# Performance work log

Hardware: AMD Instinct MI355X
Metric: run time of the kernel (lower is better)

## Reference

```python
import jax, jax.numpy as jnp
import numpy as np

S0 = 100.0
V0 = 0.04
RATE = 0.025
MC = 50000          # MC_samples; 2*MC antithetic paths
N_STEPS = 180       # == int(x[:,0].max()), pinned in setup_inputs for static shapes
WIDTH = 64
N_OPTS = 32
H = 1.0 / 360.0     # timegrid step: (maxT/360)/maxT


def setup_inputs():
    key = jax.random.key(0)
    ks = jax.random.split(key, 8)
    mat = jax.random.randint(ks[0], (N_OPTS,), 30, N_STEPS + 1).astype(jnp.float32)
    mat = mat.at[0].set(float(N_STEPS))  # pin max maturity -> static n_steps
    strikes = 80.0 + 40.0 * jax.random.uniform(ks[1], (N_OPTS,), dtype=jnp.float32)
    x = jnp.stack([mat, strikes], axis=1)  # [n_opts, 2]: (maturity_days, strike)
    z = jax.random.normal(ks[2], (MC, N_STEPS), dtype=jnp.float32)
    z1 = jax.random.normal(ks[3], (MC, N_STEPS), dtype=jnp.float32)
    # 4 stacked tiny MLPs: order = [driftS, diffusionS, driftV, diffusionV]
    W1 = 0.1 * jax.random.normal(ks[4], (4, WIDTH, 4), dtype=jnp.float32)
    b1 = jnp.zeros((4, WIDTH), jnp.float32)
    W2 = 0.1 * jax.random.normal(ks[5], (4, WIDTH, WIDTH), dtype=jnp.float32)
    b2 = jnp.zeros((4, WIDTH), jnp.float32)
    Wo = 0.05 * jax.random.normal(ks[6], (4, 1, WIDTH), dtype=jnp.float32)
    bo = jnp.zeros((4, 1), jnp.float32)
    return dict(x=x, z=z, z1=z1, W1=W1, b1=b1, W2=W2, b2=b2, Wo=Wo, bo=bo)


def _mlp4(inp, W1, b1, W2, b2, Wo, bo):
    # Evaluate the 4 tiny MLPs on the shared input [M,4] in one batched pass.
    h1 = jax.nn.relu(jnp.einsum('nwd,md->nmw', W1, inp) + b1[:, None, :])
    h2 = jax.nn.relu(jnp.einsum('nvw,nmw->nmv', W2, h1) + b2[:, None, :])
    out = jnp.einsum('now,nmw->nmo', Wo, h2) + bo[:, None, :]
    return out[..., 0]  # [4, M]


def _forward(x, z, z1, W1, b1, W2, b2, Wo, bo, remat=False):
    M = 2 * MC
    h = jnp.float32(H)
    sqh = jnp.sqrt(h)
    # correlated second Brownian: z1 <- -0.5*z + sqrt(0.75)*z1, then antithetic
    z1c = -0.5 * z + np.float32(np.sqrt(0.75)) * z1
    zf = jnp.concatenate([z, -z], axis=0)        # [M, T]
    z1f = jnp.concatenate([z1c, -z1c], axis=0)   # [M, T]
    tgrid = jnp.arange(N_STEPS, dtype=jnp.float32) * h  # t_{i-1}
    rate_col = jnp.full((M,), RATE, jnp.float32)

    def step(carry, xs):
        S, V = carry
        zc, z1cc, tc = xs
        dW = sqh * zc
        dW1 = sqh * z1cc
        inp = jnp.stack([jnp.full((M,), tc), S, V, rate_col], axis=1)  # [M,4]
        o = _mlp4(inp, W1, b1, W2, b2, Wo, bo)  # [4, M]
        Sn = jnp.maximum(S + o[0] * h + o[1] * dW, 0.0)   # max(., 0) clamp
        Vn = jnp.maximum(V + o[2] * h + o[3] * dW1, 0.0)
        return (Sn, Vn), Sn

    if remat:
        step = jax.checkpoint(step)
    init = (jnp.full((M,), S0, jnp.float32), jnp.full((M,), V0, jnp.float32))
    _, Spath = jax.lax.scan(step, init, (zf.T, z1f.T, tgrid))  # Spath: [T, M]
    Sample_path = jnp.concatenate([jnp.full((1, M), S0, jnp.float32), Spath], axis=0)  # [T+1, M]

    # vectorized option pricing over all rows of x
    idx = x[:, 0].astype(jnp.int32)                  # maturity index into path
    ST = Sample_path[idx]                            # [n_opts, M]
    payoff = jnp.maximum(ST - x[:, 1][:, None], 0.0)
    price = payoff.mean(axis=1) * jnp.exp(-RATE * x[:, 0] / 360.0)
    return price.reshape(-1, 1)


def reference(x, z, z1, W1, b1, W2, b2, Wo, bo):
    return _forward(x, z, z1, W1, b1, W2, b2, Wo, bo, remat=False)
```

## Files before the change

kernel.cpp:

```cpp
#include <hip/hip_runtime.h>
#include <math.h>

#define MC      50000
#define MPATHS  100000
#define NSTEPS  180
#define NOPTS   32

typedef __attribute__((ext_vector_type(8))) short short8;
typedef __attribute__((ext_vector_type(4))) float float4v;
typedef __attribute__((ext_vector_type(4))) unsigned u32x4;
typedef _Float16 half2v __attribute__((ext_vector_type(2)));
typedef unsigned u32x32 __attribute__((ext_vector_type(32)));

static __device__ __forceinline__ unsigned bf16u(float x) {
    unsigned u = __float_as_uint(x);
    return (u + 0x7fffu + ((u >> 16) & 1u)) >> 16;
}
static __device__ __forceinline__ float bf16val(float x) {
    return __uint_as_float(bf16u(x) << 16);
}
static __device__ __forceinline__ unsigned pkh2(float a, float b) {
    half2v h; h.x = (_Float16)a; h.y = (_Float16)b;
    return __builtin_bit_cast(unsigned, h);
}
static __device__ __forceinline__ unsigned pkrtz(float a, float b) {
    auto h = __builtin_amdgcn_cvt_pkrtz(a, b);
    return __builtin_bit_cast(unsigned, h);
}
static __device__ __forceinline__ float fdot2(unsigned w, unsigned h, float c) {
    return __builtin_amdgcn_fdot2(__builtin_bit_cast(half2v, w),
                                  __builtin_bit_cast(half2v, h), c, false);
}
static __device__ __forceinline__ short8 fr4(unsigned a, unsigned b,
                                             unsigned c, unsigned d) {
    union { unsigned u[4]; short8 s; } t;
    t.u[0] = a; t.u[1] = b; t.u[2] = c; t.u[3] = d;
    return t.s;
}
static __device__ __forceinline__ float4v mfma16(short8 a, short8 b, float4v c) {
    return __builtin_amdgcn_mfma_f32_16x16x32_bf16(a, b, c, 0, 0, 0);
}


__global__ void probe_mn(int* tbl) {
    const int lane = threadIdx.x;
    for (int s = lane; s < 2048; s += 64) tbl[s] = 0;
    const float4v z4 = {0.f, 0.f, 0.f, 0.f};
    for (int L = 0; L < 64; ++L)
        for (int j = 0; j < 8; ++j) {
            unsigned au[4] = {0u, 0u, 0u, 0u};
            if (lane == L) au[j >> 1] = 0x3F80u << (16 * (j & 1));
            short8 a = fr4(au[0], au[1], au[2], au[3]);
            short8 b = fr4(0x3F803F80u, 0x3F803F80u, 0x3F803F80u, 0x3F803F80u);
            float4v d = mfma16(a, b, z4);
            if ((lane & 15) == 0) {
                #pragma unroll
                for (int r = 0; r < 4; ++r)
                    if (d[r] != 0.0f) tbl[L * 8 + j] = (lane >> 4) * 4 + r;
            }
        }
    for (int L = 0; L < 64; ++L)
        for (int j = 0; j < 8; ++j) {
            unsigned bu[4] = {0u, 0u, 0u, 0u};
            if (lane == L) bu[j >> 1] = 0x3F80u << (16 * (j & 1));
            short8 a = fr4(0x3F803F80u, 0x3F803F80u, 0x3F803F80u, 0x3F803F80u);
            short8 b = fr4(bu[0], bu[1], bu[2], bu[3]);
            float4v d = mfma16(a, b, z4);
            if ((lane >> 4) == 0 && d[0] != 0.0f) tbl[1024 + L * 8 + j] = (lane & 15);
        }
}

__global__ void probe_k(int* tbl) {
    const int lane = threadIdx.x;
    const int sA = blockIdx.x;
    const float4v z4 = {0.f, 0.f, 0.f, 0.f};
    unsigned au[4] = {0u, 0u, 0u, 0u};
    if (lane == (sA >> 3)) au[(sA & 7) >> 1] = 0x3F80u << (16 * (sA & 1));
    short8 a = fr4(au[0], au[1], au[2], au[3]);
    int kid = -1;
    for (int sB = 0; sB < 512; ++sB) {
        unsigned bu[4] = {0u, 0u, 0u, 0u};
        const int LB = sB >> 3, jB = sB & 7;
        if (lane == LB) bu[jB >> 1] = 0x3F80u << (16 * (jB & 1));
        short8 b = fr4(bu[0], bu[1], bu[2], bu[3]);
        float4v d = mfma16(a, b, z4);
        bool hit = (d[0] != 0.f) | (d[1] != 0.f) | (d[2] != 0.f) | (d[3] != 0.f);
        if (__any(hit)) {
            if (kid < 0) kid = sB;
            if (lane == 0) tbl[1536 + sB] = kid;
        }
    }
    if (lane == 0) tbl[512 + sA] = (kid < 0) ? 0 : kid;
}

__global__ void finalize_verify(int* tbl, int* flag) {
    __shared__ int cnt[32];
    __shared__ int minv[32];
    const int lane = threadIdx.x;
    if (lane < 32) { cnt[lane] = 0; minv[lane] = 0; }
    int rA[8], rB[8];
    #pragma unroll
    for (int j = 0; j < 8; ++j) {
        const int s = lane * 8 + j;
        const int kidA = tbl[512 + s], kidB = tbl[1536 + s];
        int ra = 0, rb = 0;
        for (int u = 0; u < 512; ++u) {
            const int canon = (tbl[1536 + u] == u);
            ra += canon & (u < kidA);
            rb += canon & (u < kidB);
        }
        rA[j] = ra & 31; rB[j] = rb & 31;
    }
    __syncthreads();
    #pragma unroll
    for (int j = 0; j < 8; ++j) {
        tbl[512 + lane * 8 + j]  = rA[j];
        tbl[1536 + lane * 8 + j] = rB[j];
    }
    unsigned au[4] = {0u, 0u, 0u, 0u}, bu[4] = {0u, 0u, 0u, 0u};
    #pragma unroll
    for (int j = 0; j < 8; ++j) {
        const int s = lane * 8 + j;
        const int m = tbl[s] & 15, ka = rA[j];
        const int n = tbl[1024 + s] & 15, kb = rB[j];
        const int fv = ((m * 7 + ka * 3) % 5) - 2;
        const int gv = ((kb * 5 + n * 11) % 7) - 3;
        au[j >> 1] |= bf16u((float)fv) << (16 * (j & 1));
        bu[j >> 1] |= bf16u((float)gv) << (16 * (j & 1));
    }
    const float4v z4 = {0.f, 0.f, 0.f, 0.f};
    float4v d = mfma16(fr4(au[0], au[1], au[2], au[3]),
                       fr4(bu[0], bu[1], bu[2], bu[3]), z4);
    const int col = lane & 15;
    bool ok = true;
    #pragma unroll
    for (int r = 0; r < 4; ++r) {
        const int row = (lane >> 4) * 4 + r;
        int ref = 0;
        for (int k = 0; k < 32; ++k)
            ref += (((row * 7 + k * 3) % 5) - 2) * (((k * 5 + col * 11) % 7) - 3);
        ok = ok && (d[r] == (float)ref);
    }
    bool okf = ok;
    #pragma unroll
    for (int j = 0; j < 8; ++j) {
        okf = okf && ((tbl[1024 + lane * 8 + j] & 15) == (lane & 15));
        const int ref = __shfl(rB[j], lane & 48, 64);
        okf = okf && (rB[j] == ref);
    }
    if ((lane & 15) == 0) {
        const int g = lane >> 4;
        #pragma unroll
        for (int j = 0; j < 8; ++j) {
            atomicAdd(&cnt[rB[j]], 1);
            minv[rB[j]] = 16 * ((j >> 2) & 1) + 4 * g + 2 * ((j >> 1) & 1) + (j & 1);
        }
    }
    __syncthreads();
    if (lane < 32) {
        okf = okf && (cnt[lane] == 1);
        tbl[2048 + lane] = minv[lane];
    }
    const bool allok = __all(okf);
    if (lane == 0) *flag = allok ? 1 : 0;
}

__global__ void build_frags(const float* __restrict__ W1, const float* __restrict__ b1,
                            const float* __restrict__ W2, const float* __restrict__ Wo,
                            const int* __restrict__ tbl,
                            uint4* __restrict__ w1f, uint4* __restrict__ w2f,
                            uint4* __restrict__ w3f) {
    const int t = blockIdx.x * 256 + threadIdx.x;
    if (t >= 3584) return;
    const int lane = t & 63, frag = t >> 6;
    const float rateB = bf16val(0.025f);
    unsigned u[4] = {0u, 0u, 0u, 0u};
    if (frag < 16) {
        const int net = frag >> 2, mt = frag & 3;
        #pragma unroll
        for (int j = 0; j < 8; ++j) {
            const int s = lane * 8 + j;
            const int m = tbl[s] & 15, k = tbl[512 + s] & 31;
            unsigned bits = 0u;
            if (k < 12) {
                const int kk = (k < 6) ? k : k - 6;
                const int M = net * 64 + 16 * mt + m;
                float v;
                if (kk == 0)                 v = W1[M * 4 + 0];
                else if (kk == 1 || kk == 4) v = W1[M * 4 + 1];
                else if (kk == 2 || kk == 5) v = W1[M * 4 + 2];
                else                         v = W1[M * 4 + 3] + b1[M] / rateB;
                bits = (k < 6) ? bf16u(v) : bf16u(v - bf16val(v));
            }
            u[j >> 1] |= bits << (16 * (j & 1));
        }
        w1f[frag * 64 + lane] = make_uint4(u[0], u[1], u[2], u[3]);
    } else if (frag < 48) {
        const int f2 = frag - 16;
        const int net = f2 >> 3, mt = (f2 >> 1) & 3, kc = f2 & 1;
        #pragma unroll
        for (int j = 0; j < 8; ++j) {
            const int s = lane * 8 + j;
            const int m = tbl[s] & 15, k = tbl[512 + s] & 31;
            const float v = W2[(net * 64 + 16 * mt + m) * 64 + 32 * kc + tbl[2048 + k]];
            u[j >> 1] |= bf16u(v) << (16 * (j & 1));
        }
        w2f[f2 * 64 + lane] = make_uint4(u[0], u[1], u[2], u[3]);
    } else {
        const int f3 = frag - 48;
        const int net = f3 >> 1, kc = f3 & 1;
        #pragma unroll
        for (int j = 0; j < 8; ++j) {
            const int s = lane * 8 + j;
            const int k = tbl[512 + s] & 31;
            const float v = Wo[net * 64 + 32 * kc + tbl[2048 + k]];
            u[j >> 1] |= bf16u(v) << (16 * (j & 1));
        }
        w3f[f3 * 64 + lane] = make_uint4(u[0], u[1], u[2], u[3]);
    }
}

__global__ __launch_bounds__(256, 3)
void sde_mfma_w4(const float* __restrict__ x, const float* __restrict__ z,
                 const float* __restrict__ z1, const float* __restrict__ b2,
                 const float* __restrict__ bo,
                 const int* __restrict__ tbl, const uint4* __restrict__ w1f,
                 const uint4* __restrict__ w2f, const uint4* __restrict__ w3f,
                 const int* __restrict__ flag, float* __restrict__ acc)
{
    if (*flag != 1) return;
    __shared__ __align__(16) float b2_s[256];
    __shared__ float dxch[2][4][64];
    __shared__ float ls_k[NOPTS];
    __shared__ int   maskTab[NSTEPS + 4];

    const int tid = threadIdx.x;
    const int wv = tid >> 6, lane = tid & 63;
    const int q = lane >> 4, c = lane & 15;

    for (int j = tid; j < 256; j += 256) b2_s[j] = b2[j];
    for (int j = tid; j < NSTEPS + 4; j += 256) maskTab[j] = 0;
    if (tid < NOPTS) ls_k[tid] = x[2 * tid + 1];
    __syncthreads();
    if (tid < NOPTS) atomicOr(&maskTab[(int)x[2 * tid]], 1 << tid);
    __syncthreads();

    const unsigned rate16 = bf16u(0.025f);
    unsigned selAB[4], dynM[4], cU[4], mT[4];
    {
        int rowj[8];
        #pragma unroll
        for (int j = 0; j < 8; ++j) {
            const int kb = tbl[1536 + lane * 8 + j] & 31;
            rowj[j] = (kb < 6) ? kb : ((kb < 12) ? kb - 6 : 6);
        }
        #pragma unroll
        for (int w = 0; w < 4; ++w) {
            unsigned s = 0, d = 0, cu = 0, mt_ = 0;
            #pragma unroll
            for (int h = 0; h < 2; ++h) {
                const int r = rowj[2 * w + h];
                unsigned hs = 0x0504u, hd = 0u, hcu = 0u, hmt = 0u;
                if      (r == 1) { hs = 0x0504u; hd = 0xFFFFu; }
                else if (r == 2) { hs = 0x0706u; hd = 0xFFFFu; }
                else if (r == 4) { hs = 0x0100u; hd = 0xFFFFu; }
                else if (r == 5) { hs = 0x0302u; hd = 0xFFFFu; }
                else if (r == 0) { hmt = 0xFFFFu; }
                else if (r == 3) { hcu = rate16; }
                s  |= hs  << (16 * h); d   |= hd  << (16 * h);
                cu |= hcu << (16 * h); mt_ |= hmt << (16 * h);
            }
            selAB[w] = s; dynM[w] = d; cU[w] = cu; mT[w] = mt_;
        }
    }

    const int p_ = blockIdx.x * 64 + lane;
    const float wgt = (p_ < MPATHS) ? 1.0f : 0.0f;
    int pc = (p_ < MPATHS) ? p_ : (MPATHS - 1);
    float sgn = 1.0f; int row_ = pc;
    if (pc >= MC) { sgn = -1.0f; row_ -= MC; }
    const float* __restrict__ zrow  = z  + (size_t)row_ * NSTEPS;
    const float* __restrict__ z1row = z1 + (size_t)row_ * NSTEPS;

    const float hh = 1.0f / 360.0f, sqh = sqrtf(hh);
    const float s75 = 0.86602540378443864676f;
    const float bon = bo[wv];

    const u32x4* __restrict__ w1v = (const u32x4*)w1f;
    const u32x4* __restrict__ w2v = (const u32x4*)w2f;
    const u32x4* __restrict__ w3v = (const u32x4*)w3f;
    u32x4 a1v[4], a2v[8];
    #pragma unroll
    for (int mt = 0; mt < 4; ++mt) {
        a1v[mt]         = w1v[(wv * 4 + mt) * 64 + lane];
        a2v[2 * mt]     = w2v[((wv * 4 + mt) * 2 + 0) * 64 + lane];
        a2v[2 * mt + 1] = w2v[((wv * 4 + mt) * 2 + 1) * 64 + lane];
    }
    const u32x4 a3v0 = w3v[(wv * 2 + 0) * 64 + lane];
    const u32x4 a3v1 = w3v[(wv * 2 + 1) * 64 + lane];
    float4v c4r[4];
    #pragma unroll
    for (int mt = 0; mt < 4; ++mt)
        c4r[mt] = *(const float4v*)&b2_s[wv * 64 + 16 * mt + 4 * q];

    float S = 100.0f, V = 0.04f;

    const bool needZ  = (wv == 1) | (wv == 3);
    const bool needZ1 = (wv == 3);
    float4 zc = {0.f, 0.f, 0.f, 0.f}, z1c = {0.f, 0.f, 0.f, 0.f};
    float4 zn = zc, z1n = z1c;
    if (needZ)  zc  = *(const float4*)(zrow);
    if (needZ1) z1c = *(const float4*)(z1row);

    #pragma unroll 1
    for (int ch = 0; ch < NSTEPS / 4; ++ch) {
        if (ch + 1 < NSTEPS / 4) {
            if (needZ)  zn  = *(const float4*)(zrow  + 4 * (ch + 1));
            if (needZ1) z1n = *(const float4*)(z1row + 4 * (ch + 1));
        }
        #pragma unroll
        for (int ii = 0; ii < 4; ++ii) {
            const int i = 4 * ch + ii;
            const float zz  = (ii == 0) ? zc.x  : (ii == 1) ? zc.y  : (ii == 2) ? zc.z  : zc.w;
            const float zz1 = (ii == 0) ? z1c.x : (ii == 1) ? z1c.y : (ii == 2) ? z1c.z : z1c.w;
            float mult;
            if      (wv == 1) mult = sqh * (sgn * zz);
            else if (wv == 3) mult = sqh * (sgn * (-0.5f * zz + s75 * zz1));
            else              mult = hh;

            const float t = (float)i * hh;
            const unsigned tB = bf16u(t);
            const unsigned tB2 = tB | (tB << 16);
            unsigned UW[4];
            #pragma unroll
            for (int w = 0; w < 4; ++w) UW[w] = cU[w] | (mT[w] & tB2);

            const unsigned Shu = bf16u(S), Vhu = bf16u(V);
            const unsigned PA = Shu | (Vhu << 16);
            const float Sr = S - __uint_as_float(Shu << 16);
            const float Vr = V - __uint_as_float(Vhu << 16);
            const unsigned PB = __builtin_amdgcn_perm(__float_as_uint(Vr),
                                                      __float_as_uint(Sr), 0x07060302u);

            float osel = 0.0f;
            #pragma unroll
            for (int nt = 0; nt < 4; ++nt) {
                const int a = (nt << 6) | (c << 2);
                const unsigned Ap = (unsigned)__builtin_amdgcn_ds_bpermute(a, (int)PA);
                const unsigned Bp = (unsigned)__builtin_amdgcn_ds_bpermute(a, (int)PB);
                u32x4 b1v;
                b1v.x = (__builtin_amdgcn_perm(Ap, Bp, selAB[0]) & dynM[0]) | UW[0];
                b1v.y = (__builtin_amdgcn_perm(Ap, Bp, selAB[1]) & dynM[1]) | UW[1];
                b1v.z = (__builtin_amdgcn_perm(Ap, Bp, selAB[2]) & dynM[2]) | UW[2];
                b1v.w = (__builtin_amdgcn_perm(Ap, Bp, selAB[3]) & dynM[3]) | UW[3];
                const short8 B1s = __builtin_bit_cast(short8, b1v);

                const float4v z4 = {0.f, 0.f, 0.f, 0.f};
                u32x4 bk0, bk1;
                #pragma unroll
                for (int mt = 0; mt < 4; ++mt) {
                    float4v d = mfma16(__builtin_bit_cast(short8, a1v[mt]), B1s, z4);
                    const unsigned r0 = __float_as_uint(fmaxf(d[0], 0.f));
                    const unsigned r1 = __float_as_uint(fmaxf(d[1], 0.f));
                    const unsigned r2 = __float_as_uint(fmaxf(d[2], 0.f));
                    const unsigned r3 = __float_as_uint(fmaxf(d[3], 0.f));
                    const unsigned plo = __builtin_amdgcn_perm(r1, r0, 0x07060302u);
                    const unsigned phi = __builtin_amdgcn_perm(r3, r2, 0x07060302u);
                    if      (mt == 0) { bk0.x = plo; bk0.y = phi; }
                    else if (mt == 1) { bk0.z = plo; bk0.w = phi; }
                    else if (mt == 2) { bk1.x = plo; bk1.y = phi; }
                    else              { bk1.z = plo; bk1.w = phi; }
                }
                const short8 Bk0 = __builtin_bit_cast(short8, bk0);
                const short8 Bk1 = __builtin_bit_cast(short8, bk1);
                u32x4 hk0, hk1;
                #pragma unroll
                for (int mt = 0; mt < 4; ++mt) {
                    float4v d = mfma16(__builtin_bit_cast(short8, a2v[2 * mt]), Bk0, c4r[mt]);
                    d = mfma16(__builtin_bit_cast(short8, a2v[2 * mt + 1]), Bk1, d);
                    const unsigned r0 = __float_as_uint(fmaxf(d[0], 0.f));
                    const unsigned r1 = __float_as_uint(fmaxf(d[1], 0.f));
                    const unsigned r2 = __float_as_uint(fmaxf(d[2], 0.f));
                    const unsigned r3 = __float_as_uint(fmaxf(d[3], 0.f));
                    const unsigned plo = __builtin_amdgcn_perm(r1, r0, 0x07060302u);
                    const unsigned phi = __builtin_amdgcn_perm(r3, r2, 0x07060302u);
                    if      (mt == 0) { hk0.x = plo; hk0.y = phi; }
                    else if (mt == 1) { hk0.z = plo; hk0.w = phi; }
                    else if (mt == 2) { hk1.x = plo; hk1.y = phi; }
                    else              { hk1.z = plo; hk1.w = phi; }
                }
                float4v dO = mfma16(__builtin_bit_cast(short8, a3v0),
                                    __builtin_bit_cast(short8, hk0), z4);
                dO = mfma16(__builtin_bit_cast(short8, a3v1),
                            __builtin_bit_cast(short8, hk1), dO);
                if (nt == q) osel = dO[0];
            }
            const float o = osel + bon;

            dxch[i & 1][wv][lane] = o * mult;
            __syncthreads();
            const float dS = dxch[i & 1][0][lane] + dxch[i & 1][1][lane];
            const float dV = dxch[i & 1][2][lane] + dxch[i & 1][3][lane];
            S = fmaxf(S + dS, 0.0f);
            V = fmaxf(V + dV, 0.0f);

            if (wv == 0) {
                int mm = maskTab[i + 1];
                while (mm) {
                    const int qq = __ffs(mm) - 1; mm &= mm - 1;
                    float pay = wgt * fmaxf(S - ls_k[qq], 0.0f);
                    #pragma unroll
                    for (int off = 32; off > 0; off >>= 1)
                        pay += __shfl_down(pay, off, 64);
                    if (lane == 0) atomicAdd(&acc[qq], pay);
                }
            }
        }
        zc = zn; z1c = z1n;
    }
}

__global__ void pack_w(const float* __restrict__ W1, const float* __restrict__ W2,
                       unsigned* __restrict__ wp1, unsigned* __restrict__ wp2) {
    int i = blockIdx.x * 256 + threadIdx.x;
    if (i < 512)              wp1[i] = pkh2(W1[2 * i], W1[2 * i + 1]);
    else if (i < 512 + 8192) { int k = i - 512; wp2[k] = pkh2(W2[2 * k], W2[2 * k + 1]); }
}

__global__ __launch_bounds__(64, 2)
void sde_dot2(const float* __restrict__ x, const float* __restrict__ z,
              const float* __restrict__ z1, const float* __restrict__ b1,
              const float* __restrict__ b2, const float* __restrict__ Wo,
              const float* __restrict__ bo, const uint4* __restrict__ wp1,
              const uint4* __restrict__ wp2, const int* __restrict__ flag,
              float* __restrict__ acc)
{
    if (*flag == 1) return;
    __shared__ __align__(16) uint4 wlds[2176];
    __shared__ float ls_k[NOPTS];
    __shared__ int   maskTab[NSTEPS + 4];
    const int tid = threadIdx.x;
    for (int j = tid; j < 2176; j += 64) wlds[j] = (j < 128) ? wp1[j] : wp2[j - 128];
    for (int jj = tid; jj < NSTEPS + 4; jj += 64) maskTab[jj] = 0;
    if (tid < NOPTS) ls_k[tid] = x[2 * tid + 1];
    __syncthreads();
    if (tid < NOPTS) atomicOr(&maskTab[(int)x[2 * tid]], 1 << tid);
    __syncthreads();
    const int pA = blockIdx.x * 128 + tid, pB = pA + 64;
    const float wgtA = (pA < MPATHS) ? 1.0f : 0.0f;
    const float wgtB = (pB < MPATHS) ? 1.0f : 0.0f;
    int pcA = (pA < MPATHS) ? pA : (MPATHS - 1);
    int pcB = (pB < MPATHS) ? pB : (MPATHS - 1);
    float sgnA = 1.0f, sgnB = 1.0f; int rowA = pcA, rowB = pcB;
    if (pcA >= MC) { sgnA = -1.0f; rowA -= MC; }
    if (pcB >= MC) { sgnB = -1.0f; rowB -= MC; }
    const float* __restrict__ zA  = z  + (size_t)rowA * NSTEPS;
    const float* __restrict__ z1A = z1 + (size_t)rowA * NSTEPS;
    const float* __restrict__ zB  = z  + (size_t)rowB * NSTEPS;
    const float* __restrict__ z1B = z1 + (size_t)rowB * NSTEPS;
    const float hh = 1.0f / 360.0f, sqh = sqrtf(hh);
    const float s75 = 0.86602540378443864676f, rate = 0.025f;
    float SA = 100.0f, VA = 0.04f, SB = 100.0f, VB = 0.04f;
    #pragma unroll 1
    for (int i = 0; i < NSTEPS; ++i) {
        const float zcrA = zA[i], z1rA = z1A[i], zcrB = zB[i], z1rB = z1B[i];
        const float dWA = sqh * (sgnA * zcrA);
        const float dW1A = sqh * (sgnA * (-0.5f * zcrA + s75 * z1rA));
        const float dWB = sqh * (sgnB * zcrB);
        const float dW1B = sqh * (sgnB * (-0.5f * zcrB + s75 * z1rB));
        const float t = (float)i * hh;
        const unsigned inA01 = pkrtz(t, SA), inA23 = pkrtz(VA, rate);
        const unsigned inB01 = pkrtz(t, SB), inB23 = pkrtz(VB, rate);
        float dSA = 0.f, dVA = 0.f, dSB = 0.f, dVB = 0.f;
        #pragma unroll 1
        for (int net = 0; net < 4; ++net) {
            const float* __restrict__ b1n = b1 + net * 64;
            const float* __restrict__ b2n = b2 + net * 64;
            const float* __restrict__ won = Wo + net * 64;
            const uint4* __restrict__ wl1 = &wlds[net * 32];
            const uint4* __restrict__ wl2 = &wlds[128 + net * 512];
            u32x32 hA, hB;
            #pragma unroll
            for (int u = 0; u < 64; u += 2) {
                const uint4 wv = wl1[u >> 1];
                const float bb0 = b1n[u], bb1 = b1n[u + 1];
                float a0 = fdot2(wv.x, inA01, bb0); a0 = fdot2(wv.y, inA23, a0);
                float a1 = fdot2(wv.z, inA01, bb1); a1 = fdot2(wv.w, inA23, a1);
                float c0 = fdot2(wv.x, inB01, bb0); c0 = fdot2(wv.y, inB23, c0);
                float c1 = fdot2(wv.z, inB01, bb1); c1 = fdot2(wv.w, inB23, c1);
                hA[u >> 1] = pkrtz(fmaxf(a0, 0.f), fmaxf(a1, 0.f));
                hB[u >> 1] = pkrtz(fmaxf(c0, 0.f), fmaxf(c1, 0.f));
            }
            float outA = bo[net], outB = outA;
            #pragma unroll 1
            for (int j = 0; j < 64; j += 4) {
                const uint4* __restrict__ r0 = wl2 + (j + 0) * 8;
                const uint4* __restrict__ r1 = wl2 + (j + 1) * 8;
                const uint4* __restrict__ r2 = wl2 + (j + 2) * 8;
                const uint4* __restrict__ r3 = wl2 + (j + 3) * 8;
                float a0 = b2n[j], a1 = b2n[j + 1], a2 = b2n[j + 2], a3 = b2n[j + 3];
                float c0 = a0, c1 = a1, c2 = a2, c3 = a3;
                #pragma unroll
                for (int kk = 0; kk < 8; ++kk) {
                    const uint4 w0 = r0[kk], w1 = r1[kk], w2 = r2[kk], w3 = r3[kk];
                    const unsigned hA0 = hA[4 * kk], hA1 = hA[4 * kk + 1];
                    const unsigned hA2 = hA[4 * kk + 2], hA3 = hA[4 * kk + 3];
                    const unsigned hB0 = hB[4 * kk], hB1 = hB[4 * kk + 1];
                    const unsigned hB2 = hB[4 * kk + 2], hB3 = hB[4 * kk + 3];
                    a0 = fdot2(w0.x, hA0, a0); a0 = fdot2(w0.y, hA1, a0);
                    a0 = fdot2(w0.z, hA2, a0); a0 = fdot2(w0.w, hA3, a0);
                    a1 = fdot2(w1.x, hA0, a1); a1 = fdot2(w1.y, hA1, a1);
                    a1 = fdot2(w1.z, hA2, a1); a1 = fdot2(w1.w, hA3, a1);
                    a2 = fdot2(w2.x, hA0, a2); a2 = fdot2(w2.y, hA1, a2);
                    a2 = fdot2(w2.z, hA2, a2); a2 = fdot2(w2.w, hA3, a2);
                    a3 = fdot2(w3.x, hA0, a3); a3 = fdot2(w3.y, hA1, a3);
                    a3 = fdot2(w3.z, hA2, a3); a3 = fdot2(w3.w, hA3, a3);
                    c0 = fdot2(w0.x, hB0, c0); c0 = fdot2(w0.y, hB1, c0);
                    c0 = fdot2(w0.z, hB2, c0); c0 = fdot2(w0.w, hB3, c0);
                    c1 = fdot2(w1.x, hB0, c1); c1 = fdot2(w1.y, hB1, c1);
                    c1 = fdot2(w1.z, hB2, c1); c1 = fdot2(w1.w, hB3, c1);
                    c2 = fdot2(w2.x, hB0, c2); c2 = fdot2(w2.y, hB1, c2);
                    c2 = fdot2(w2.z, hB2, c2); c2 = fdot2(w2.w, hB3, c2);
                    c3 = fdot2(w3.x, hB0, c3); c3 = fdot2(w3.y, hB1, c3);
                    c3 = fdot2(w3.z, hB2, c3); c3 = fdot2(w3.w, hB3, c3);
                }
                const float wo0 = won[j], wo1 = won[j + 1];
                const float wo2 = won[j + 2], wo3 = won[j + 3];
                outA = fmaf(wo0, fmaxf(a0, 0.f), outA); outA = fmaf(wo1, fmaxf(a1, 0.f), outA);
                outA = fmaf(wo2, fmaxf(a2, 0.f), outA); outA = fmaf(wo3, fmaxf(a3, 0.f), outA);
                outB = fmaf(wo0, fmaxf(c0, 0.f), outB); outB = fmaf(wo1, fmaxf(c1, 0.f), outB);
                outB = fmaf(wo2, fmaxf(c2, 0.f), outB); outB = fmaf(wo3, fmaxf(c3, 0.f), outB);
            }
            const float msA = (net == 0) ? hh : (net == 1) ? dWA  : 0.0f;
            const float mvA = (net == 2) ? hh : (net == 3) ? dW1A : 0.0f;
            const float msB = (net == 0) ? hh : (net == 1) ? dWB  : 0.0f;
            const float mvB = (net == 2) ? hh : (net == 3) ? dW1B : 0.0f;
            dSA = fmaf(outA, msA, dSA); dVA = fmaf(outA, mvA, dVA);
            dSB = fmaf(outB, msB, dSB); dVB = fmaf(outB, mvB, dVB);
        }
        SA = fmaxf(SA + dSA, 0.f); VA = fmaxf(VA + dVA, 0.f);
        SB = fmaxf(SB + dSB, 0.f); VB = fmaxf(VB + dVB, 0.f);
        int mm = maskTab[i + 1];
        while (mm) {
            const int qq = __ffs(mm) - 1; mm &= mm - 1;
            float pay = wgtA * fmaxf(SA - ls_k[qq], 0.f) + wgtB * fmaxf(SB - ls_k[qq], 0.f);
            #pragma unroll
            for (int off = 32; off > 0; off >>= 1)
                pay += __shfl_down(pay, off, 64);
            if (tid == 0) atomicAdd(&acc[qq], pay);
        }
    }
}

__global__ void price_kernel(const float* __restrict__ x, const float* __restrict__ acc,
                             float* __restrict__ out) {
    const int q = threadIdx.x;
    if (q < NOPTS) {
        const float mat = x[q * 2];
        out[q] = acc[q] * (1.0f / (float)MPATHS) * expf((-0.025f * mat) / 360.0f);
    }
}

extern "C" void kernel_launch(void* const* d_in, const int* in_sizes, int n_in,
                              void* d_out, int out_size, void* d_ws, size_t ws_size,
                              hipStream_t stream)
{
    const float* x  = (const float*)d_in[0];
    const float* z  = (const float*)d_in[1];
    const float* z1 = (const float*)d_in[2];
    const float* W1 = (const float*)d_in[3];
    const float* b1 = (const float*)d_in[4];
    const float* W2 = (const float*)d_in[5];
    const float* b2 = (const float*)d_in[6];
    const float* Wo = (const float*)d_in[7];
    const float* bo = (const float*)d_in[8];

    char* ws = (char*)d_ws;
    float*    acc  = (float*)ws;
    int*      flag = (int*)(ws + 256);
    int*      tbl  = (int*)(ws + 1024);
    uint4*    w1f  = (uint4*)(ws + 16384);
    uint4*    w2f  = (uint4*)(ws + 32768);
    unsigned* wp1  = (unsigned*)(ws + 65536);
    unsigned* wp2  = wp1 + 512;
    uint4*    w3f  = (uint4*)(ws + 100352);

    (void)hipMemsetAsync(acc, 0, NOPTS * sizeof(float), stream);
    pack_w<<<(512 + 8192 + 255) / 256, 256, 0, stream>>>(W1, W2, wp1, wp2);
    probe_mn<<<1, 64, 0, stream>>>(tbl);
    probe_k<<<512, 64, 0, stream>>>(tbl);
    finalize_verify<<<1, 64, 0, stream>>>(tbl, flag);
    build_frags<<<14, 256, 0, stream>>>(W1, b1, W2, Wo, tbl, w1f, w2f, w3f);

    const int gridS = (MPATHS + 63) / 64;
    sde_mfma_w4<<<gridS, 256, 0, stream>>>(x, z, z1, b2, bo, tbl, w1f, w2f, w3f,
                                           flag, acc);
    const int gridF = (MPATHS + 127) / 128;
    sde_dot2<<<gridF, 64, 0, stream>>>(x, z, z1, b1, b2, Wo, bo,
                                       (const uint4*)wp1, (const uint4*)wp2, flag, acc);
    price_kernel<<<1, 64, 0, stream>>>(x, acc, (float*)d_out);
}
```

Baseline: 1.491 ms.

## Split MLP nets across two waves per block instead of four

Each block now runs 128 threads, and each wave evaluates two of the four MLP nets (drift and diffusion for S, or for V) rather than one net per wave. The combined increment is formed locally with an fma, and only two values are exchanged through shared memory per step. Weight fragments for layers 1 and 2 are now reloaded from global memory inside the step loop instead of being held in registers. This aims to cut barrier and cross-wave exchange cost and lower register pressure, at the cost of repeated weight loads and twice the serial MFMA work per wave.

```diff
diff --git a/kernel.cpp b/kernel.cpp
--- a/kernel.cpp
+++ b/kernel.cpp
@@ -220,8 +220,8 @@
     }
 }
 
-__global__ __launch_bounds__(256, 3)
-void sde_mfma_w4(const float* __restrict__ x, const float* __restrict__ z,
+__global__ __launch_bounds__(128, 3)
+void sde_mfma_p2(const float* __restrict__ x, const float* __restrict__ z,
                  const float* __restrict__ z1, const float* __restrict__ b2,
                  const float* __restrict__ bo,
                  const int* __restrict__ tbl, const uint4* __restrict__ w1f,
@@ -230,7 +230,7 @@
 {
     if (*flag != 1) return;
     __shared__ __align__(16) float b2_s[256];
-    __shared__ float dxch[2][4][64];
+    __shared__ float dxch[2][2][64];
     __shared__ float ls_k[NOPTS];
     __shared__ int   maskTab[NSTEPS + 4];
 
@@ -238,8 +238,8 @@
     const int wv = tid >> 6, lane = tid & 63;
     const int q = lane >> 4, c = lane & 15;
 
-    for (int j = tid; j < 256; j += 256) b2_s[j] = b2[j];
-    for (int j = tid; j < NSTEPS + 4; j += 256) maskTab[j] = 0;
+    for (int j = tid; j < 256; j += 128) b2_s[j] = b2[j];
+    for (int j = tid; j < NSTEPS + 4; j += 128) maskTab[j] = 0;
     if (tid < NOPTS) ls_k[tid] = x[2 * tid + 1];
     __syncthreads();
     if (tid < NOPTS) atomicOr(&maskTab[(int)x[2 * tid]], 1 << tid);
@@ -284,38 +284,27 @@
 
     const float hh = 1.0f / 360.0f, sqh = sqrtf(hh);
     const float s75 = 0.86602540378443864676f;
-    const float bon = bo[wv];
+    const float bo0 = bo[2 * wv], bo1 = bo[2 * wv + 1];
 
     const u32x4* __restrict__ w1v = (const u32x4*)w1f;
     const u32x4* __restrict__ w2v = (const u32x4*)w2f;
     const u32x4* __restrict__ w3v = (const u32x4*)w3f;
-    u32x4 a1v[4], a2v[8];
+    u32x4 a3[4];
     #pragma unroll
-    for (int mt = 0; mt < 4; ++mt) {
-        a1v[mt]         = w1v[(wv * 4 + mt) * 64 + lane];
-        a2v[2 * mt]     = w2v[((wv * 4 + mt) * 2 + 0) * 64 + lane];
-        a2v[2 * mt + 1] = w2v[((wv * 4 + mt) * 2 + 1) * 64 + lane];
-    }
-    const u32x4 a3v0 = w3v[(wv * 2 + 0) * 64 + lane];
-    const u32x4 a3v1 = w3v[(wv * 2 + 1) * 64 + lane];
-    float4v c4r[4];
-    #pragma unroll
-    for (int mt = 0; mt < 4; ++mt)
-        c4r[mt] = *(const float4v*)&b2_s[wv * 64 + 16 * mt + 4 * q];
+    for (int f = 0; f < 4; ++f) a3[f] = w3v[(wv * 4 + f) * 64 + lane];
 
     float S = 100.0f, V = 0.04f;
 
-    const bool needZ  = (wv == 1) | (wv == 3);
-    const bool needZ1 = (wv == 3);
-    float4 zc = {0.f, 0.f, 0.f, 0.f}, z1c = {0.f, 0.f, 0.f, 0.f};
+    const bool needZ1 = (wv == 1);
+    float4 zc  = *(const float4*)(zrow);
+    float4 z1c = {0.f, 0.f, 0.f, 0.f};
+    if (needZ1) z1c = *(const float4*)(z1row);
     float4 zn = zc, z1n = z1c;
-    if (needZ)  zc  = *(const float4*)(zrow);
-    if (needZ1) z1c = *(const float4*)(z1row);
 
     #pragma unroll 1
     for (int ch = 0; ch < NSTEPS / 4; ++ch) {
         if (ch + 1 < NSTEPS / 4) {
-            if (needZ)  zn  = *(const float4*)(zrow  + 4 * (ch + 1));
+            zn = *(const float4*)(zrow + 4 * (ch + 1));
             if (needZ1) z1n = *(const float4*)(z1row + 4 * (ch + 1));
         }
         #pragma unroll
@@ -323,10 +312,9 @@
             const int i = 4 * ch + ii;
             const float zz  = (ii == 0) ? zc.x  : (ii == 1) ? zc.y  : (ii == 2) ? zc.z  : zc.w;
             const float zz1 = (ii == 0) ? z1c.x : (ii == 1) ? z1c.y : (ii == 2) ? z1c.z : z1c.w;
-            float mult;
-            if      (wv == 1) mult = sqh * (sgn * zz);
-            else if (wv == 3) mult = sqh * (sgn * (-0.5f * zz + s75 * zz1));
-            else              mult = hh;
+            float m1;
+            if (wv) m1 = sqh * (sgn * (-0.5f * zz + s75 * zz1));
+            else    m1 = sqh * (sgn * zz);
 
             const float t = (float)i * hh;
             const unsigned tB = bf16u(t);
@@ -342,7 +330,7 @@
             const unsigned PB = __builtin_amdgcn_perm(__float_as_uint(Vr),
                                                       __float_as_uint(Sr), 0x07060302u);
 
-            float osel = 0.0f;
+            float osel0 = 0.0f, osel1 = 0.0f;
             #pragma unroll
             for (int nt = 0; nt < 4; ++nt) {
                 const int a = (nt << 6) | (c << 2);
@@ -354,53 +342,64 @@
                 b1v.z = (__builtin_amdgcn_perm(Ap, Bp, selAB[2]) & dynM[2]) | UW[2];
                 b1v.w = (__builtin_amdgcn_perm(Ap, Bp, selAB[3]) & dynM[3]) | UW[3];
                 const short8 B1s = __builtin_bit_cast(short8, b1v);
-
                 const float4v z4 = {0.f, 0.f, 0.f, 0.f};
-                u32x4 bk0, bk1;
+
                 #pragma unroll
-                for (int mt = 0; mt < 4; ++mt) {
-                    float4v d = mfma16(__builtin_bit_cast(short8, a1v[mt]), B1s, z4);
-                    const unsigned r0 = __float_as_uint(fmaxf(d[0], 0.f));
-                    const unsigned r1 = __float_as_uint(fmaxf(d[1], 0.f));
-                    const unsigned r2 = __float_as_uint(fmaxf(d[2], 0.f));
-                    const unsigned r3 = __float_as_uint(fmaxf(d[3], 0.f));
-                    const unsigned plo = __builtin_amdgcn_perm(r1, r0, 0x07060302u);
-                    const unsigned phi = __builtin_amdgcn_perm(r3, r2, 0x07060302u);
-                    if      (mt == 0) { bk0.x = plo; bk0.y = phi; }
-                    else if (mt == 1) { bk0.z = plo; bk0.w = phi; }
-                    else if (mt == 2) { bk1.x = plo; bk1.y = phi; }
-                    else              { bk1.z = plo; bk1.w = phi; }
+                for (int j2 = 0; j2 < 2; ++j2) {
+                    const int net = 2 * wv + j2;
+                    u32x4 bk0, bk1;
+                    #pragma unroll
+                    for (int mt = 0; mt < 4; ++mt) {
+                        const u32x4 f1 = w1v[(net * 4 + mt) * 64 + lane];
+                        float4v d = mfma16(__builtin_bit_cast(short8, f1), B1s, z4);
+                        const unsigned r0 = __float_as_uint(fmaxf(d[0], 0.f));
+                        const unsigned r1 = __float_as_uint(fmaxf(d[1], 0.f));
+                        const unsigned r2 = __float_as_uint(fmaxf(d[2], 0.f));
+                        const unsigned r3 = __float_as_uint(fmaxf(d[3], 0.f));
+                        const unsigned plo = __builtin_amdgcn_perm(r1, r0, 0x07060302u);
+                        const unsigned phi = __builtin_amdgcn_perm(r3, r2, 0x07060302u);
+                        if      (mt == 0) { bk0.x = plo; bk0.y = phi; }
+                        else if (mt == 1) { bk0.z = plo; bk0.w = phi; }
+                        else if (mt == 2) { bk1.x = plo; bk1.y = phi; }
+                        else              { bk1.z = plo; bk1.w = phi; }
+                    }
+                    const short8 Bk0 = __builtin_bit_cast(short8, bk0);
+                    const short8 Bk1 = __builtin_bit_cast(short8, bk1);
+                    u32x4 hk0, hk1;
+                    #pragma unroll
+                    for (int mt = 0; mt < 4; ++mt) {
+                        const u32x4 f2a = w2v[((net * 4 + mt) * 2 + 0) * 64 + lane];
+                        const u32x4 f2b = w2v[((net * 4 + mt) * 2 + 1) * 64 + lane];
+                        const float4v cc = *(const float4v*)&b2_s[net * 64 + 16 * mt + 4 * q];
+                        float4v d = mfma16(__builtin_bit_cast(short8, f2a), Bk0, cc);
+                        d = mfma16(__builtin_bit_cast(short8, f2b), Bk1, d);
+                        const unsigned r0 = __float_as_uint(fmaxf(d[0], 0.f));
+                        const unsigned r1 = __float_as_uint(fmaxf(d[1], 0.f));
+                        const unsigned r2 = __float_as_uint(fmaxf(d[2], 0.f));
+                        const unsigned r3 = __float_as_uint(fmaxf(d[3], 0.f));
+                        const unsigned plo = __builtin_amdgcn_perm(r1, r0, 0x07060302u);
+                        const unsigned phi = __builtin_amdgcn_perm(r3, r2, 0x07060302u);
+                        if      (mt == 0) { hk0.x = plo; hk0.y = phi; }
+                        else if (mt == 1) { hk0.z = plo; hk0.w = phi; }
+                        else if (mt == 2) { hk1.x = plo; hk1.y = phi; }
+                        else              { hk1.z = plo; hk1.w = phi; }
+                    }
+                    const float4v z40 = {0.f, 0.f, 0.f, 0.f};
+                    float4v dO = mfma16(__builtin_bit_cast(short8, a3[j2 * 2]),
+                                        __builtin_bit_cast(short8, hk0), z40);
+                    dO = mfma16(__builtin_bit_cast(short8, a3[j2 * 2 + 1]),
+                                __builtin_bit_cast(short8, hk1), dO);
+                    if (nt == q) { if (j2 == 0) osel0 = dO[0]; else osel1 = dO[0]; }
                 }
-                const short8 Bk0 = __builtin_bit_cast(short8, bk0);
-                const short8 Bk1 = __builtin_bit_cast(short8, bk1);
-                u32x4 hk0, hk1;
-                #pragma unroll
-                for (int mt = 0; mt < 4; ++mt) {
-                    float4v d = mfma16(__builtin_bit_cast(short8, a2v[2 * mt]), Bk0, c4r[mt]);
-                    d = mfma16(__builtin_bit_cast(short8, a2v[2 * mt + 1]), Bk1, d);
-                    const unsigned r0 = __float_as_uint(fmaxf(d[0], 0.f));
-                    const unsigned r1 = __float_as_uint(fmaxf(d[1], 0.f));
-                    const unsigned r2 = __float_as_uint(fmaxf(d[2], 0.f));
-                    const unsigned r3 = __float_as_uint(fmaxf(d[3], 0.f));
-                    const unsigned plo = __builtin_amdgcn_perm(r1, r0, 0x07060302u);
-                    const unsigned phi = __builtin_amdgcn_perm(r3, r2, 0x07060302u);
-                    if      (mt == 0) { hk0.x = plo; hk0.y = phi; }
-                    else if (mt == 1) { hk0.z = plo; hk0.w = phi; }
-                    else if (mt == 2) { hk1.x = plo; hk1.y = phi; }
-                    else              { hk1.z = plo; hk1.w = phi; }
-                }
-                float4v dO = mfma16(__builtin_bit_cast(short8, a3v0),
-                                    __builtin_bit_cast(short8, hk0), z4);
-                dO = mfma16(__builtin_bit_cast(short8, a3v1),
-                            __builtin_bit_cast(short8, hk1), dO);
-                if (nt == q) osel = dO[0];
             }
-            const float o = osel + bon;
-
-            dxch[i & 1][wv][lane] = o * mult;
+            const float o0 = osel0 + bo0;
+            const float o1 = osel1 + bo1;
+            const float dX = fmaf(o1, m1, o0 * hh);
+
+            dxch[i & 1][wv][lane] = dX;
             __syncthreads();
-            const float dS = dxch[i & 1][0][lane] + dxch[i & 1][1][lane];
-            const float dV = dxch[i & 1][2][lane] + dxch[i & 1][3][lane];
+            const float dS = dxch[i & 1][0][lane];
+            const float dV = dxch[i & 1][1][lane];
             S = fmaxf(S + dS, 0.0f);
             V = fmaxf(V + dV, 0.0f);
 
@@ -593,7 +592,7 @@
     build_frags<<<14, 256, 0, stream>>>(W1, b1, W2, Wo, tbl, w1f, w2f, w3f);
 
     const int gridS = (MPATHS + 63) / 64;
-    sde_mfma_w4<<<gridS, 256, 0, stream>>>(x, z, z1, b2, bo, tbl, w1f, w2f, w3f,
+    sde_mfma_p2<<<gridS, 128, 0, stream>>>(x, z, z1, b2, bo, tbl, w1f, w2f, w3f,
                                            flag, acc);
     const int gridF = (MPATHS + 127) / 128;
     sde_dot2<<<gridF, 64, 0, stream>>>(x, z, z1, b1, b2, Wo, bo,
```

Result: slower. 5.810 ms (+289.7%).
